# Kernel optimization log

Measured on AMD Instinct MI355X. Metric: run time of the kernel, lower is better.

## Reference

```python
import jax, jax.numpy as jnp
import numpy as np

N, E = 12288, 196608
IN_DIM, HID, HEADS, EMB, K = 128, 256, 4, 16, 2
NEG_SLOPE = 0.2


def gat_layer(x, src, dst, W, a_s, a_d, b, heads, out_dim):
    # x: [N, Fin]; src/dst: [E'] (self-loops already appended)
    n = x.shape[0]
    h = (x @ W).reshape(n, heads, out_dim)                 # [N,H,F]
    alpha_src = jnp.einsum('nhf,hf->nh', h, a_s)           # [N,H]
    alpha_dst = jnp.einsum('nhf,hf->nh', h, a_d)
    e = jax.nn.leaky_relu(alpha_src[src] + alpha_dst[dst], NEG_SLOPE)  # [E,H]
    # softmax over incoming edges per destination node
    m = jax.ops.segment_max(e, dst, num_segments=n)
    ex = jnp.exp(e - m[dst])
    s = jax.ops.segment_sum(ex, dst, num_segments=n)
    alpha = ex / s[dst]                                    # [E,H]
    msg = h[src] * alpha[..., None]                        # [E,H,F]
    agg = jax.ops.segment_sum(msg, dst, num_segments=n)    # [N,H,F]
    return agg.reshape(n, heads * out_dim) + b


def setup_inputs() -> dict:
    key = jax.random.key(0)
    ks = jax.random.split(key, 16)
    x = jax.random.normal(ks[0], (N, IN_DIM), dtype=jnp.float32)
    edge_index = jax.random.randint(ks[1], (2, E), 0, N, dtype=jnp.int32)

    def glorot(k, shape):
        fan = shape[0] + shape[-1]
        return jax.random.normal(k, shape, dtype=jnp.float32) * jnp.sqrt(2.0 / fan)

    inp = {"x": x, "edge_index": edge_index}
    inp["W1"] = glorot(ks[2], (IN_DIM, HEADS * HID))
    inp["as1"] = glorot(ks[3], (HEADS, HID))
    inp["ad1"] = glorot(ks[4], (HEADS, HID))
    inp["b1"] = jnp.zeros((HEADS * HID,), jnp.float32)
    inp["W2"] = glorot(ks[5], (HEADS * HID, HEADS * HID))
    inp["as2"] = glorot(ks[6], (HEADS, HID))
    inp["ad2"] = glorot(ks[7], (HEADS, HID))
    inp["b2"] = jnp.zeros((HEADS * HID,), jnp.float32)
    # layer 3: 1024 -> 16, 1 head
    inp["W3"] = glorot(ks[8], (HEADS * HID, EMB))
    inp["as3"] = glorot(ks[9], (1, EMB))
    inp["ad3"] = glorot(ks[10], (1, EMB))
    inp["b3"] = jnp.zeros((EMB,), jnp.float32)
    inp["centers"] = jax.random.normal(ks[11], (K, EMB), dtype=jnp.float32)
    return inp


def reference(x, edge_index, W1, as1, ad1, b1, W2, as2, ad2, b2, W3, as3, ad3, b3, centers):
    n = x.shape[0]
    loop = jnp.arange(n, dtype=edge_index.dtype)
    src = jnp.concatenate([edge_index[0], loop])
    dst = jnp.concatenate([edge_index[1], loop])

    h = jax.nn.elu(gat_layer(x, src, dst, W1, as1, ad1, b1, HEADS, HID))
    h = jax.nn.elu(gat_layer(h, src, dst, W2, as2, ad2, b2, HEADS, HID))
    z = gat_layer(h, src, dst, W3, as3, ad3, b3, 1, EMB)   # [N,EMB]

    adj_recon = jax.nn.sigmoid(z @ z.T)                    # [N,N]

    # Student-t soft assignment
    d2 = jnp.sum((z[:, None, :] - centers[None, :, :]) ** 2, axis=2)  # [N,K]
    q = 1.0 / (1.0 + d2)
    q = q / jnp.sum(q, axis=1, keepdims=True)
    return z, adj_recon, q
```

## Files before the change

kernel.cpp:

```cpp
#include <hip/hip_runtime.h>
#include <hip/hip_bf16.h>
#include <math.h>

#define N_NODES 12288
#define N_EDGES 196608
#define EP_EDGES (N_EDGES + N_NODES)
#define HEADS 4
#define HID 256
#define FDIM 1024
#define EMB 16
#define NEG_SLOPE 0.2f

typedef __attribute__((ext_vector_type(8))) short short8;
typedef __attribute__((ext_vector_type(4))) float f32x4;
typedef __attribute__((ext_vector_type(2))) float f32x2;

__device__ __forceinline__ unsigned short f2bf(float f) {
  unsigned int u = __float_as_uint(f);
  u = (u + 0x7FFFu + ((u >> 16) & 1u)) >> 16;
  return (unsigned short)u;
}
__device__ __forceinline__ float bf2f(unsigned short h) {
  return __uint_as_float(((unsigned int)h) << 16);
}

__device__ __forceinline__ void t_tile_hi(const float* __restrict__ W,
                                          unsigned short* __restrict__ Th,
                                          int K, int N, int k0, int n0,
                                          int t, float (*tile)[33]) {
  int rr = t >> 3, cc = (t & 7) * 4;
  float4 v = *reinterpret_cast<const float4*>(&W[(size_t)(k0 + rr) * N + n0 + cc]);
  tile[rr][cc + 0] = v.x; tile[rr][cc + 1] = v.y; tile[rr][cc + 2] = v.z; tile[rr][cc + 3] = v.w;
  __syncthreads();
  ushort4 h;
  h.x = f2bf(tile[cc + 0][rr]);
  h.y = f2bf(tile[cc + 1][rr]);
  h.z = f2bf(tile[cc + 2][rr]);
  h.w = f2bf(tile[cc + 3][rr]);
  *reinterpret_cast<ushort4*>(&Th[(size_t)(n0 + rr) * K + k0 + cc]) = h;
}

#define HIST_BLKS (EP_EDGES / 256)
__global__ __launch_bounds__(256) void k_hist_prep(const int* __restrict__ ei,
                                                   int* __restrict__ cnt,
                                                   const float* __restrict__ x,
                                                   unsigned short* __restrict__ xbf,
                                                   const float* __restrict__ W1,
                                                   unsigned short* __restrict__ w1tHi,
                                                   const float* __restrict__ W2,
                                                   unsigned short* __restrict__ w2tHi,
                                                   const float* __restrict__ as1,
                                                   const float* __restrict__ ad1,
                                                   float* __restrict__ wa,
                                                   const float* __restrict__ W3,
                                                   unsigned short* __restrict__ w3t) {
  __shared__ float tile[32][33];
  int b = blockIdx.x, t = threadIdx.x;
  if (b < HIST_BLKS) {
    int i = b * 256 + t;
    if (i < EP_EDGES) {
      int d = (i < N_EDGES) ? ei[N_EDGES + i] : (i - N_EDGES);
      atomicAdd(&cnt[d], 1);
    }
  } else if (b < HIST_BLKS + 1536) {
    int i = (b - HIST_BLKS) * 256 + t;
    float4 v = *reinterpret_cast<const float4*>(&x[(size_t)i * 4]);
    ushort4 h;
    h.x = f2bf(v.x); h.y = f2bf(v.y); h.z = f2bf(v.z); h.w = f2bf(v.w);
    *reinterpret_cast<ushort4*>(&xbf[(size_t)i * 4]) = h;
  } else if (b < HIST_BLKS + 1536 + 128) {
    int tt = b - HIST_BLKS - 1536;
    t_tile_hi(W1, w1tHi, 128, FDIM, (tt >> 5) * 32, (tt & 31) * 32, t, tile);
  } else if (b < HIST_BLKS + 1536 + 128 + 1024) {
    int tt = b - HIST_BLKS - 1536 - 128;
    t_tile_hi(W2, w2tHi, FDIM, FDIM, (tt >> 5) * 32, (tt & 31) * 32, t, tile);
  } else if (b == HIST_BLKS + 1536 + 128 + 1024) {
    for (int idx = t; idx < 1024; idx += 256) {
      int sd = idx >> 9, h = (idx >> 7) & 3, k = idx & 127;
      const float* av = sd ? ad1 : as1;
      float acc = 0.f;
      for (int f = 0; f < 256; ++f)
        acc = fmaf(W1[(size_t)k * FDIM + h * 256 + f], av[h * 256 + f], acc);
      wa[idx] = acc;
    }
  } else {
    for (int idx = t; idx < 16384; idx += 256) {
      int c = idx >> 10, k = idx & 1023;
      w3t[idx] = f2bf(W3[(size_t)k * 16 + c]);
    }
  }
}

__global__ __launch_bounds__(1024) void k_scan_alpha(const int* __restrict__ cnt,
                                                     int* __restrict__ row_ptr,
                                                     int* __restrict__ bsum,
                                                     const float* __restrict__ x,
                                                     const float* __restrict__ wa,
                                                     float* __restrict__ asrc,
                                                     float* __restrict__ adst) {
  __shared__ int sd[1024];
  int tid = threadIdx.x;
  if (blockIdx.x < 12) {
    int gid = blockIdx.x * 1024 + tid;
    int v = cnt[gid];
    sd[tid] = v;
    __syncthreads();
    for (int d = 1; d < 1024; d <<= 1) {
      int t2 = (tid >= d) ? sd[tid - d] : 0;
      __syncthreads();
      sd[tid] += t2;
      __syncthreads();
    }
    row_ptr[gid] = sd[tid] - v;
    if (tid == 1023) bsum[blockIdx.x] = sd[1023];
  } else {
    int id = (blockIdx.x - 12) * 1024 + tid;
    int n = id >> 2, h = id & 3;
    const float* wsv = wa + h * 128;
    const float* wdv = wa + 512 + h * 128;
    const float* xr = x + (size_t)n * 128;
    float accs = 0.f, accd = 0.f;
#pragma unroll
    for (int k = 0; k < 128; k += 4) {
      float4 xv = *reinterpret_cast<const float4*>(&xr[k]);
      float4 s4 = *reinterpret_cast<const float4*>(&wsv[k]);
      float4 d4 = *reinterpret_cast<const float4*>(&wdv[k]);
      accs = fmaf(xv.x, s4.x, fmaf(xv.y, s4.y, fmaf(xv.z, s4.z, fmaf(xv.w, s4.w, accs))));
      accd = fmaf(xv.x, d4.x, fmaf(xv.y, d4.y, fmaf(xv.z, d4.z, fmaf(xv.w, d4.w, accd))));
    }
    asrc[n * 4 + h] = accs;
    adst[n * 4 + h] = accd;
  }
}

__global__ void k_scan23(int* __restrict__ row_ptr, const int* __restrict__ bsum) {
  int gid = blockIdx.x * 256 + threadIdx.x;
  int blk = gid >> 10;
  int boffv = 0;
  for (int j = 0; j < blk; ++j) boffv += bsum[j];
  row_ptr[gid] += boffv;
  if (gid == 0) {
    int tot = 0;
    for (int j = 0; j < 12; ++j) tot += bsum[j];
    row_ptr[N_NODES] = tot;
  }
}

__global__ void k_scatter(const int* __restrict__ ei, const int* __restrict__ row_ptr,
                          int* __restrict__ cur, int* __restrict__ csr_src) {
  int i = blockIdx.x * 256 + threadIdx.x;
  if (i >= EP_EDGES) return;
  int s, d;
  if (i < N_EDGES) { s = ei[i]; d = ei[N_EDGES + i]; }
  else             { s = i - N_EDGES; d = s; }
  int pos = row_ptr[d] + atomicAdd(&cur[d], 1);
  csr_src[pos] = s;
}

__global__ __launch_bounds__(256) void k_aggx(const unsigned short* __restrict__ xbf,
                                              const float* __restrict__ asrc,
                                              const float* __restrict__ adst,
                                              const int* __restrict__ row_ptr,
                                              const int* __restrict__ csr_src,
                                              unsigned short* __restrict__ outHi) {
  int node = (blockIdx.x * 256 + threadIdx.x) >> 6;
  int lane = threadIdx.x & 63;
  int beg = row_ptr[node], end = row_ptr[node + 1];
  float4 adn = *reinterpret_cast<const float4*>(&adst[node * 4]);
  float m0 = -INFINITY, m1 = -INFINITY, m2 = -INFINITY, m3 = -INFINITY;
  float s0 = 0.f, s1 = 0.f, s2 = 0.f, s3 = 0.f;
  float a0x = 0.f, a0y = 0.f, a1x = 0.f, a1y = 0.f;
  float a2x = 0.f, a2y = 0.f, a3x = 0.f, a3y = 0.f;
  for (int e = beg; e < end; ++e) {
    int sidx = csr_src[e];
    float4 av = *reinterpret_cast<const float4*>(&asrc[sidx * 4]);
    ushort2 hu = *reinterpret_cast<const ushort2*>(&xbf[(size_t)sidx * 128 + lane * 2]);
    float hx = bf2f(hu.x), hy = bf2f(hu.y);
    float a, nm, sc, p;
    a = av.x + adn.x; a = a > 0.f ? a : NEG_SLOPE * a;
    nm = fmaxf(m0, a); sc = __expf(m0 - nm); p = __expf(a - nm); m0 = nm;
    s0 = s0 * sc + p; a0x = a0x * sc + p * hx; a0y = a0y * sc + p * hy;
    a = av.y + adn.y; a = a > 0.f ? a : NEG_SLOPE * a;
    nm = fmaxf(m1, a); sc = __expf(m1 - nm); p = __expf(a - nm); m1 = nm;
    s1 = s1 * sc + p; a1x = a1x * sc + p * hx; a1y = a1y * sc + p * hy;
    a = av.z + adn.z; a = a > 0.f ? a : NEG_SLOPE * a;
    nm = fmaxf(m2, a); sc = __expf(m2 - nm); p = __expf(a - nm); m2 = nm;
    s2 = s2 * sc + p; a2x = a2x * sc + p * hx; a2y = a2y * sc + p * hy;
    a = av.w + adn.w; a = a > 0.f ? a : NEG_SLOPE * a;
    nm = fmaxf(m3, a); sc = __expf(m3 - nm); p = __expf(a - nm); m3 = nm;
    s3 = s3 * sc + p; a3x = a3x * sc + p * hx; a3y = a3y * sc + p * hy;
  }
  size_t base = (size_t)node * 512 + lane * 2;
  ushort2 o;
  float inv;
  inv = 1.f / s0; o.x = f2bf(a0x * inv); o.y = f2bf(a0y * inv);
  *reinterpret_cast<ushort2*>(&outHi[base + 0 * 128]) = o;
  inv = 1.f / s1; o.x = f2bf(a1x * inv); o.y = f2bf(a1y * inv);
  *reinterpret_cast<ushort2*>(&outHi[base + 1 * 128]) = o;
  inv = 1.f / s2; o.x = f2bf(a2x * inv); o.y = f2bf(a2y * inv);
  *reinterpret_cast<ushort2*>(&outHi[base + 2 * 128]) = o;
  inv = 1.f / s3; o.x = f2bf(a3x * inv); o.y = f2bf(a3y * inv);
  *reinterpret_cast<ushort2*>(&outHi[base + 3 * 128]) = o;
}

template <int MODE>
__global__ __launch_bounds__(256) void k_gemm(const unsigned short* __restrict__ A,
                                              const unsigned short* __restrict__ B,
                                              unsigned short* __restrict__ Out,
                                              const float* __restrict__ bias,
                                              const float* __restrict__ a_s,
                                              const float* __restrict__ a_d,
                                              float* __restrict__ asrcP,
                                              float* __restrict__ adstP,
                                              int M, int N, int K, int lda) {
  __shared__ unsigned short sA[128 * 32], sB[128 * 32];
  const int tid = threadIdx.x;
  const int lane = tid & 63, wv = tid >> 6;
  const int row0 = blockIdx.y * 128, col0 = blockIdx.x * 128;
  const int mBase = (wv >> 1) * 64, nBase = (wv & 1) * 64;
  const int lane15 = lane & 15;
  const int aoff = (MODE == 1) ? (col0 >> 8) * 128 : 0;

  f32x4 acc[4][4];
#pragma unroll
  for (int m = 0; m < 4; ++m)
#pragma unroll
    for (int n = 0; n < 4; ++n) acc[m][n] = (f32x4){0.f, 0.f, 0.f, 0.f};

  int rS[2], cS[2], dS[2];
#pragma unroll
  for (int c = 0; c < 2; ++c) {
    int p = c * 4096 + tid * 16;
    int r = p >> 6, u = (p >> 4) & 3;
    int f = (r & 3) ^ ((r >> 2) & 3);
    rS[c] = r; cS[c] = (u ^ f) * 8; dS[c] = c * 2048 + tid * 8;
  }
  const int fR = (lane & 3) ^ ((lane >> 2) & 3);
  const int uprime = (((lane >> 4) ^ fR) * 8);

  for (int k0 = 0; k0 < K; k0 += 32) {
#pragma unroll
    for (int c = 0; c < 2; ++c) {
      size_t ga = (size_t)(row0 + rS[c]) * lda + aoff + k0 + cS[c];
      size_t gb = (size_t)(col0 + rS[c]) * K + k0 + cS[c];
      __builtin_amdgcn_global_load_lds((const __attribute__((address_space(1))) void*)(A + ga),
                                       (__attribute__((address_space(3))) void*)(sA + dS[c]), 16, 0, 0);
      __builtin_amdgcn_global_load_lds((const __attribute__((address_space(1))) void*)(B + gb),
                                       (__attribute__((address_space(3))) void*)(sB + dS[c]), 16, 0, 0);
    }
    __syncthreads();

    short8 a[4], b[4];
#pragma unroll
    for (int m = 0; m < 4; ++m) {
      int ia = (mBase + m * 16 + lane15) * 32 + uprime;
      a[m] = *reinterpret_cast<const short8*>(sA + ia);
      int ib = (nBase + m * 16 + lane15) * 32 + uprime;
      b[m] = *reinterpret_cast<const short8*>(sB + ib);
    }
#pragma unroll
    for (int m = 0; m < 4; ++m)
#pragma unroll
      for (int n = 0; n < 4; ++n)
        acc[m][n] = __builtin_amdgcn_mfma_f32_16x16x32_bf16(a[m], b[n], acc[m][n], 0, 0, 0);
    __syncthreads();
  }

  const int head = col0 >> 8;
  const int q = ((col0 >> 6) & 2) | (nBase >> 6);
  float asv[4], adv[4];
  if (MODE == 0) {
#pragma unroll
    for (int n = 0; n < 4; ++n) {
      int cc = col0 + nBase + n * 16 + lane15;
      asv[n] = a_s[cc];
      adv[n] = a_d[cc];
    }
  }

#pragma unroll
  for (int m = 0; m < 4; ++m) {
    int rr = row0 + mBase + m * 16 + (lane >> 4) * 4;
#pragma unroll
    for (int j = 0; j < 4; ++j) {
      if (MODE == 1) {
#pragma unroll
        for (int n = 0; n < 4; ++n) {
          int cc = col0 + nBase + n * 16 + lane15;
          float v = acc[m][n][j] + bias[cc];
          v = v > 0.f ? v : __expf(v) - 1.f;
          Out[(size_t)(rr + j) * N + cc] = f2bf(v);
        }
      } else {
        float ps = 0.f, pd = 0.f;
#pragma unroll
        for (int n = 0; n < 4; ++n) {
          int cc = col0 + nBase + n * 16 + lane15;
          float v = acc[m][n][j];
          Out[(size_t)(rr + j) * N + cc] = f2bf(v);
          ps = fmaf(v, asv[n], ps);
          pd = fmaf(v, adv[n], pd);
        }
        ps += __shfl_xor(ps, 1); pd += __shfl_xor(pd, 1);
        ps += __shfl_xor(ps, 2); pd += __shfl_xor(pd, 2);
        ps += __shfl_xor(ps, 4); pd += __shfl_xor(pd, 4);
        ps += __shfl_xor(ps, 8); pd += __shfl_xor(pd, 8);
        if (lane15 == 0) {
          asrcP[(size_t)(rr + j) * 16 + head * 4 + q] = ps;
          adstP[(size_t)(rr + j) * 16 + head * 4 + q] = pd;
        }
      }
    }
  }
}

__global__ void k_repack8(const unsigned short* __restrict__ hbf,
                          unsigned int* __restrict__ h8) {
  int i = blockIdx.x * 256 + threadIdx.x;
  ushort4 v = *reinterpret_cast<const ushort4*>(&hbf[(size_t)i * 4]);
  int w = __builtin_amdgcn_cvt_pk_fp8_f32(bf2f(v.x), bf2f(v.y), 0, false);
  w = __builtin_amdgcn_cvt_pk_fp8_f32(bf2f(v.z), bf2f(v.w), w, true);
  h8[i] = (unsigned int)w;
}

__global__ __launch_bounds__(256) void k_agg4(const unsigned int* __restrict__ h8,
                                              const float* __restrict__ asrcP,
                                              const float* __restrict__ adstP,
                                              const int* __restrict__ row_ptr,
                                              const int* __restrict__ csr_src, const float* __restrict__ bias,
                                              unsigned short* __restrict__ outHi) {
  int wid = (blockIdx.x * 256 + threadIdx.x) >> 6;
  int lane = threadIdx.x & 63;
  int node = wid >> 2, hd = wid & 3;
  int beg = row_ptr[node], end = row_ptr[node + 1];
  float4 dq = *reinterpret_cast<const float4*>(&adstP[(size_t)node * 16 + hd * 4]);
  float adn = dq.x + dq.y + dq.z + dq.w;
  float m = -INFINITY, s = 0.f;
  float ax = 0.f, ay = 0.f, az = 0.f, aw = 0.f;
  for (int e = beg; e < end; ++e) {
    int sidx = csr_src[e];
    float4 sq = *reinterpret_cast<const float4*>(&asrcP[(size_t)sidx * 16 + hd * 4]);
    float a = (sq.x + sq.y + sq.z + sq.w) + adn;
    a = a > 0.f ? a : NEG_SLOPE * a;
    float nm = fmaxf(m, a);
    float sc = __expf(m - nm);
    float p  = __expf(a - nm);
    m = nm;
    s = s * sc + p;
    unsigned int dw = h8[(size_t)sidx * 256 + hd * 64 + lane];
    f32x2 lo = __builtin_amdgcn_cvt_pk_f32_fp8(dw, false);
    f32x2 hi = __builtin_amdgcn_cvt_pk_f32_fp8(dw, true);
    ax = ax * sc + p * lo.x;
    ay = ay * sc + p * lo.y;
    az = az * sc + p * hi.x;
    aw = aw * sc + p * hi.y;
  }
  float inv = 1.f / s;
  int fo = hd * HID + lane * 4;
  float4 bv = *reinterpret_cast<const float4*>(&bias[fo]);
  float4 o;
  o.x = ax * inv + bv.x; o.y = ay * inv + bv.y; o.z = az * inv + bv.z; o.w = aw * inv + bv.w;
  o.x = o.x > 0.f ? o.x : __expf(o.x) - 1.f;
  o.y = o.y > 0.f ? o.y : __expf(o.y) - 1.f;
  o.z = o.z > 0.f ? o.z : __expf(o.z) - 1.f;
  o.w = o.w > 0.f ? o.w : __expf(o.w) - 1.f;
  ushort4 hh;
  hh.x = f2bf(o.x); hh.y = f2bf(o.y); hh.z = f2bf(o.z); hh.w = f2bf(o.w);
  *reinterpret_cast<ushort4*>(&outHi[(size_t)node * FDIM + fo]) = hh;
}

__global__ __launch_bounds__(256) void k_gemm_n16(const unsigned short* __restrict__ A,
                                                  const unsigned short* __restrict__ w3t,
                                                  const float* __restrict__ a_s,
                                                  const float* __restrict__ a_d,
                                                  float* __restrict__ C,
                                                  float* __restrict__ asrc,
                                                  float* __restrict__ adst) {
  int wave = (blockIdx.x * 256 + threadIdx.x) >> 6;
  int lane = threadIdx.x & 63;
  int lane15 = lane & 15;
  int row0 = wave * 16;
  int kg = (lane >> 4) * 8;
  f32x4 acc = (f32x4){0.f, 0.f, 0.f, 0.f};
  const unsigned short* Ar = A + (size_t)(row0 + lane15) * FDIM + kg;
  const unsigned short* Br = w3t + (size_t)lane15 * FDIM + kg;
  for (int k0 = 0; k0 < FDIM; k0 += 32) {
    short8 a = *reinterpret_cast<const short8*>(Ar + k0);
    short8 b = *reinterpret_cast<const short8*>(Br + k0);
    acc = __builtin_amdgcn_mfma_f32_16x16x32_bf16(a, b, acc, 0, 0, 0);
  }
  float asv = a_s[lane15], adv = a_d[lane15];
  int rbase = row0 + (lane >> 4) * 4;
#pragma unroll
  for (int j = 0; j < 4; ++j) {
    float v = acc[j];
    C[(size_t)(rbase + j) * EMB + lane15] = v;
    float ps = v * asv, pd = v * adv;
    ps += __shfl_xor(ps, 1); pd += __shfl_xor(pd, 1);
    ps += __shfl_xor(ps, 2); pd += __shfl_xor(pd, 2);
    ps += __shfl_xor(ps, 4); pd += __shfl_xor(pd, 4);
    ps += __shfl_xor(ps, 8); pd += __shfl_xor(pd, 8);
    if (lane15 == 0) { asrc[rbase + j] = ps; adst[rbase + j] = pd; }
  }
}

__global__ __launch_bounds__(256) void k_agg1(const float* __restrict__ h3, const float* __restrict__ asrc,
                                              const float* __restrict__ adst, const int* __restrict__ row_ptr,
                                              const int* __restrict__ csr_src, const float* __restrict__ bias,
                                              const float* __restrict__ centers,
                                              float* __restrict__ z, float* __restrict__ qout,
                                              unsigned short* __restrict__ zh,
                                              unsigned short* __restrict__ zl) {
  int idx = blockIdx.x * 256 + threadIdx.x;
  int node = idx >> 4, f = idx & 15;
  if (node >= N_NODES) return;
  int beg = row_ptr[node], end = row_ptr[node + 1];
  float adn = adst[node];
  float m = -INFINITY, s = 0.f, acc = 0.f;
  for (int e = beg; e < end; ++e) {
    int sidx = csr_src[e];
    float a = asrc[sidx] + adn;
    a = a > 0.f ? a : NEG_SLOPE * a;
    float nm = fmaxf(m, a);
    float sc = __expf(m - nm);
    float p  = __expf(a - nm);
    m = nm;
    s = s * sc + p;
    acc = acc * sc + p * h3[sidx * EMB + f];
  }
  float zv = acc / s + bias[f];
  z[node * EMB + f] = zv;
  unsigned short hv = f2bf(zv);
  zh[node * EMB + f] = hv;
  zl[node * EMB + f] = f2bf(zv - bf2f(hv));
  float d0 = zv - centers[f];       d0 *= d0;
  float d1 = zv - centers[EMB + f]; d1 *= d1;
  d0 += __shfl_xor(d0, 1); d1 += __shfl_xor(d1, 1);
  d0 += __shfl_xor(d0, 2); d1 += __shfl_xor(d1, 2);
  d0 += __shfl_xor(d0, 4); d1 += __shfl_xor(d1, 4);
  d0 += __shfl_xor(d0, 8); d1 += __shfl_xor(d1, 8);
  if (f == 0) {
    float q0 = 1.f / (1.f + d0), q1 = 1.f / (1.f + d1);
    float inv = 1.f / (q0 + q1);
    qout[node * 2 + 0] = q0 * inv;
    qout[node * 2 + 1] = q1 * inv;
  }
}

__global__ __launch_bounds__(256) void k_adj(const unsigned short* __restrict__ zh,
                                             const unsigned short* __restrict__ zl,
                                             float* __restrict__ adj) {
  int tid = threadIdx.x;
  int lane = tid & 63, wv = tid >> 6;
  int r0 = blockIdx.y * 128 + wv * 32, c0 = blockIdx.x * 128;
  int l15 = lane & 15, kg = lane >> 4;
  short8 zero = (short8){0, 0, 0, 0, 0, 0, 0, 0};
  short8 ah[2], al[2];
#pragma unroll
  for (int g = 0; g < 2; ++g) {
    int row = r0 + g * 16 + l15;
    if (kg < 2) {
      ah[g] = *reinterpret_cast<const short8*>(&zh[(size_t)row * EMB + kg * 8]);
      al[g] = *reinterpret_cast<const short8*>(&zl[(size_t)row * EMB + kg * 8]);
    } else { ah[g] = zero; al[g] = zero; }
  }
  short8 bh[8], bl[8];
#pragma unroll
  for (int n = 0; n < 8; ++n) {
    int col = c0 + n * 16 + l15;
    if (kg < 2) {
      bh[n] = *reinterpret_cast<const short8*>(&zh[(size_t)col * EMB + kg * 8]);
      bl[n] = *reinterpret_cast<const short8*>(&zl[(size_t)col * EMB + kg * 8]);
    } else { bh[n] = zero; bl[n] = zero; }
  }
#pragma unroll
  for (int g = 0; g < 2; ++g) {
    int rbase = r0 + g * 16 + kg * 4;
#pragma unroll
    for (int n = 0; n < 8; ++n) {
      f32x4 acc = (f32x4){0.f, 0.f, 0.f, 0.f};
      acc = __builtin_amdgcn_mfma_f32_16x16x32_bf16(ah[g], bh[n], acc, 0, 0, 0);
      acc = __builtin_amdgcn_mfma_f32_16x16x32_bf16(ah[g], bl[n], acc, 0, 0, 0);
      acc = __builtin_amdgcn_mfma_f32_16x16x32_bf16(al[g], bh[n], acc, 0, 0, 0);
      int cc = c0 + n * 16 + l15;
#pragma unroll
      for (int j = 0; j < 4; ++j) {
        float v = 1.f / (1.f + __expf(-acc[j]));
        adj[(size_t)(rbase + j) * N_NODES + cc] = v;
      }
    }
  }
}

extern "C" void kernel_launch(void* const* d_in, const int* in_sizes, int n_in,
                              void* d_out, int out_size, void* d_ws, size_t ws_size,
                              hipStream_t stream) {
  const float* x   = (const float*)d_in[0];
  const int*   ei  = (const int*)d_in[1];
  const float* W1  = (const float*)d_in[2];
  const float* as1 = (const float*)d_in[3];
  const float* ad1 = (const float*)d_in[4];
  const float* b1  = (const float*)d_in[5];
  const float* W2  = (const float*)d_in[6];
  const float* as2 = (const float*)d_in[7];
  const float* ad2 = (const float*)d_in[8];
  const float* b2  = (const float*)d_in[9];
  const float* W3  = (const float*)d_in[10];
  const float* as3 = (const float*)d_in[11];
  const float* ad3 = (const float*)d_in[12];
  const float* b3  = (const float*)d_in[13];
  const float* centers = (const float*)d_in[14];
  float* out = (float*)d_out;

  char* ws = (char*)d_ws;
  size_t off = 0;
  auto alloc = [&](size_t bytes) { void* p = ws + off; off = (off + bytes + 255) & ~(size_t)255; return p; };
  int* cnt       = (int*)alloc((size_t)N_NODES * 4);
  int* cur       = (int*)alloc((size_t)N_NODES * 4);
  int* row_ptr   = (int*)alloc((size_t)(N_NODES + 1) * 4);
  int* bsum      = (int*)alloc(64 * 4);
  int* csr_src   = (int*)alloc((size_t)EP_EDGES * 4);
  float* asrcA   = (float*)alloc((size_t)N_NODES * HEADS * 4);
  float* adstA   = (float*)alloc((size_t)N_NODES * HEADS * 4);
  float* asrcP   = (float*)alloc((size_t)N_NODES * 16 * 4);
  float* adstP   = (float*)alloc((size_t)N_NODES * 16 * 4);
  float* asrc3   = (float*)alloc((size_t)N_NODES * 4);
  float* adst3   = (float*)alloc((size_t)N_NODES * 4);
  float* wa      = (float*)alloc(1024 * 4);
  unsigned short* xbf    = (unsigned short*)alloc((size_t)N_NODES * 128 * 2);
  unsigned short* aggxHi = (unsigned short*)alloc((size_t)N_NODES * 512 * 2);
  unsigned short* h1bf   = (unsigned short*)alloc((size_t)N_NODES * FDIM * 2);
  unsigned short* hbf    = (unsigned short*)alloc((size_t)N_NODES * FDIM * 2);
  unsigned int*   h8     = (unsigned int*)alloc((size_t)N_NODES * FDIM);
  unsigned short* agg2Hi = (unsigned short*)alloc((size_t)N_NODES * FDIM * 2);
  unsigned short* w1tHi  = (unsigned short*)alloc((size_t)FDIM * 128 * 2);
  unsigned short* w2tHi  = (unsigned short*)alloc((size_t)FDIM * FDIM * 2);
  unsigned short* w3t    = (unsigned short*)alloc((size_t)16 * FDIM * 2);
  unsigned short* zh     = (unsigned short*)alloc((size_t)N_NODES * EMB * 2);
  unsigned short* zl     = (unsigned short*)alloc((size_t)N_NODES * EMB * 2);
  float* bufZ    = (float*)alloc((size_t)N_NODES * EMB * 4);

  hipMemsetAsync(cnt, 0, (size_t)N_NODES * 8, stream);

  k_hist_prep<<<dim3(HIST_BLKS + 1536 + 128 + 1024 + 2), dim3(256), 0, stream>>>(
      ei, cnt, x, xbf, W1, w1tHi, W2, w2tHi, as1, ad1, wa, W3, w3t);

  k_scan_alpha<<<dim3(12 + 48), dim3(1024), 0, stream>>>(
      cnt, row_ptr, bsum, x, wa, asrcA, adstA);

  k_scan23<<<dim3(N_NODES / 256), dim3(256), 0, stream>>>(row_ptr, bsum);
  k_scatter<<<dim3((EP_EDGES + 255) / 256), dim3(256), 0, stream>>>(ei, row_ptr, cur, csr_src);

  k_aggx<<<dim3(N_NODES / 4), dim3(256), 0, stream>>>(xbf, asrcA, adstA, row_ptr, csr_src, aggxHi);
  k_gemm<1><<<dim3(FDIM / 128, N_NODES / 128), dim3(256), 0, stream>>>(
      aggxHi, w1tHi, h1bf, b1, nullptr, nullptr, nullptr, nullptr, N_NODES, FDIM, 128, 512);

  k_gemm<0><<<dim3(FDIM / 128, N_NODES / 128), dim3(256), 0, stream>>>(
      h1bf, w2tHi, hbf, nullptr, as2, ad2, asrcP, adstP, N_NODES, FDIM, FDIM, FDIM);
  k_repack8<<<dim3(N_NODES * FDIM / 4 / 256), dim3(256), 0, stream>>>(hbf, h8);
  k_agg4<<<dim3(N_NODES), dim3(256), 0, stream>>>(h8, asrcP, adstP, row_ptr, csr_src, b2, agg2Hi);

  k_gemm_n16<<<dim3(N_NODES / 64), dim3(256), 0, stream>>>(
      agg2Hi, w3t, as3, ad3, bufZ, asrc3, adst3);
  float* adj = out + (size_t)N_NODES * EMB;
  float* q   = adj + (size_t)N_NODES * N_NODES;
  k_agg1<<<dim3(N_NODES * EMB / 256), dim3(256), 0, stream>>>(
      bufZ, asrc3, adst3, row_ptr, csr_src, b3, centers, out, q, zh, zl);

  k_adj<<<dim3(N_NODES / 128, N_NODES / 128), dim3(256), 0, stream>>>(zh, zl, adj);
}
```

Measured before the change: 441.2 us.

## Fuse FP8 packing into GEMM epilogue and use two-pass softmax in aggregations

The layer-2 GEMM epilogue now shuffles accumulator values across lanes and writes FP8-packed words directly. This removes the separate bf16 output buffer and the repack kernel, saving a full write and re-read of the 12288x1024 hidden matrix. The three aggregation kernels replace online softmax with a two-pass scheme: a max pass over the edges, then a pass with one exp per edge and no rescaling. The trade-off is extra index and attention-logit gathers per edge, in exchange for fewer exps and shorter dependency chains.

New measurement: 494.1 us. 12.0% more time.

```diff
diff --git a/kernel.cpp b/kernel.cpp
--- a/kernel.cpp
+++ b/kernel.cpp
@@ -168,6 +168,15 @@
   int beg = row_ptr[node], end = row_ptr[node + 1];
   float4 adn = *reinterpret_cast<const float4*>(&adst[node * 4]);
   float m0 = -INFINITY, m1 = -INFINITY, m2 = -INFINITY, m3 = -INFINITY;
+  for (int e = beg; e < end; ++e) {
+    int sidx = csr_src[e];
+    float4 av = *reinterpret_cast<const float4*>(&asrc[sidx * 4]);
+    float a;
+    a = av.x + adn.x; a = a > 0.f ? a : NEG_SLOPE * a; m0 = fmaxf(m0, a);
+    a = av.y + adn.y; a = a > 0.f ? a : NEG_SLOPE * a; m1 = fmaxf(m1, a);
+    a = av.z + adn.z; a = a > 0.f ? a : NEG_SLOPE * a; m2 = fmaxf(m2, a);
+    a = av.w + adn.w; a = a > 0.f ? a : NEG_SLOPE * a; m3 = fmaxf(m3, a);
+  }
   float s0 = 0.f, s1 = 0.f, s2 = 0.f, s3 = 0.f;
   float a0x = 0.f, a0y = 0.f, a1x = 0.f, a1y = 0.f;
   float a2x = 0.f, a2y = 0.f, a3x = 0.f, a3y = 0.f;
@@ -176,19 +185,15 @@
     float4 av = *reinterpret_cast<const float4*>(&asrc[sidx * 4]);
     ushort2 hu = *reinterpret_cast<const ushort2*>(&xbf[(size_t)sidx * 128 + lane * 2]);
     float hx = bf2f(hu.x), hy = bf2f(hu.y);
-    float a, nm, sc, p;
+    float a, p;
     a = av.x + adn.x; a = a > 0.f ? a : NEG_SLOPE * a;
-    nm = fmaxf(m0, a); sc = __expf(m0 - nm); p = __expf(a - nm); m0 = nm;
-    s0 = s0 * sc + p; a0x = a0x * sc + p * hx; a0y = a0y * sc + p * hy;
+    p = __expf(a - m0); s0 += p; a0x = fmaf(p, hx, a0x); a0y = fmaf(p, hy, a0y);
     a = av.y + adn.y; a = a > 0.f ? a : NEG_SLOPE * a;
-    nm = fmaxf(m1, a); sc = __expf(m1 - nm); p = __expf(a - nm); m1 = nm;
-    s1 = s1 * sc + p; a1x = a1x * sc + p * hx; a1y = a1y * sc + p * hy;
+    p = __expf(a - m1); s1 += p; a1x = fmaf(p, hx, a1x); a1y = fmaf(p, hy, a1y);
     a = av.z + adn.z; a = a > 0.f ? a : NEG_SLOPE * a;
-    nm = fmaxf(m2, a); sc = __expf(m2 - nm); p = __expf(a - nm); m2 = nm;
-    s2 = s2 * sc + p; a2x = a2x * sc + p * hx; a2y = a2y * sc + p * hy;
+    p = __expf(a - m2); s2 += p; a2x = fmaf(p, hx, a2x); a2y = fmaf(p, hy, a2y);
     a = av.w + adn.w; a = a > 0.f ? a : NEG_SLOPE * a;
-    nm = fmaxf(m3, a); sc = __expf(m3 - nm); p = __expf(a - nm); m3 = nm;
-    s3 = s3 * sc + p; a3x = a3x * sc + p * hx; a3y = a3y * sc + p * hy;
+    p = __expf(a - m3); s3 += p; a3x = fmaf(p, hx, a3x); a3y = fmaf(p, hy, a3y);
   }
   size_t base = (size_t)node * 512 + lane * 2;
   ushort2 o;
@@ -206,7 +211,8 @@
 template <int MODE>
 __global__ __launch_bounds__(256) void k_gemm(const unsigned short* __restrict__ A,
                                               const unsigned short* __restrict__ B,
-                                              unsigned short* __restrict__ Out,
+                                              unsigned short* __restrict__ OutBf,
+                                              unsigned int* __restrict__ Out8,
                                               const float* __restrict__ bias,
                                               const float* __restrict__ a_s,
                                               const float* __restrict__ a_d,
@@ -289,15 +295,13 @@
           int cc = col0 + nBase + n * 16 + lane15;
           float v = acc[m][n][j] + bias[cc];
           v = v > 0.f ? v : __expf(v) - 1.f;
-          Out[(size_t)(rr + j) * N + cc] = f2bf(v);
+          OutBf[(size_t)(rr + j) * N + cc] = f2bf(v);
         }
       } else {
         float ps = 0.f, pd = 0.f;
 #pragma unroll
         for (int n = 0; n < 4; ++n) {
-          int cc = col0 + nBase + n * 16 + lane15;
           float v = acc[m][n][j];
-          Out[(size_t)(rr + j) * N + cc] = f2bf(v);
           ps = fmaf(v, asv[n], ps);
           pd = fmaf(v, adv[n], pd);
         }
@@ -309,18 +313,22 @@
           asrcP[(size_t)(rr + j) * 16 + head * 4 + q] = ps;
           adstP[(size_t)(rr + j) * 16 + head * 4 + q] = pd;
         }
+        int src = (lane & 48) | ((lane15 << 2) & 15);
+        float c0 = 0.f, c1 = 0.f, c2 = 0.f, c3 = 0.f;
+#pragma unroll
+        for (int nn = 0; nn < 4; ++nn) {
+          float t0 = __shfl(acc[m][nn][j], src + 0);
+          float t1 = __shfl(acc[m][nn][j], src + 1);
+          float t2 = __shfl(acc[m][nn][j], src + 2);
+          float t3 = __shfl(acc[m][nn][j], src + 3);
+          if ((lane15 >> 2) == nn) { c0 = t0; c1 = t1; c2 = t2; c3 = t3; }
+        }
+        int w = __builtin_amdgcn_cvt_pk_fp8_f32(c0, c1, 0, false);
+        w = __builtin_amdgcn_cvt_pk_fp8_f32(c2, c3, w, true);
+        Out8[(size_t)(rr + j) * (N >> 2) + ((col0 + nBase) >> 2) + lane15] = (unsigned int)w;
       }
     }
   }
-}
-
-__global__ void k_repack8(const unsigned short* __restrict__ hbf,
-                          unsigned int* __restrict__ h8) {
-  int i = blockIdx.x * 256 + threadIdx.x;
-  ushort4 v = *reinterpret_cast<const ushort4*>(&hbf[(size_t)i * 4]);
-  int w = __builtin_amdgcn_cvt_pk_fp8_f32(bf2f(v.x), bf2f(v.y), 0, false);
-  w = __builtin_amdgcn_cvt_pk_fp8_f32(bf2f(v.z), bf2f(v.w), w, true);
-  h8[i] = (unsigned int)w;
 }
 
 __global__ __launch_bounds__(256) void k_agg4(const unsigned int* __restrict__ h8,
@@ -335,25 +343,29 @@
   int beg = row_ptr[node], end = row_ptr[node + 1];
   float4 dq = *reinterpret_cast<const float4*>(&adstP[(size_t)node * 16 + hd * 4]);
   float adn = dq.x + dq.y + dq.z + dq.w;
-  float m = -INFINITY, s = 0.f;
-  float ax = 0.f, ay = 0.f, az = 0.f, aw = 0.f;
+  float m = -INFINITY;
   for (int e = beg; e < end; ++e) {
     int sidx = csr_src[e];
     float4 sq = *reinterpret_cast<const float4*>(&asrcP[(size_t)sidx * 16 + hd * 4]);
     float a = (sq.x + sq.y + sq.z + sq.w) + adn;
     a = a > 0.f ? a : NEG_SLOPE * a;
-    float nm = fmaxf(m, a);
-    float sc = __expf(m - nm);
-    float p  = __expf(a - nm);
-    m = nm;
-    s = s * sc + p;
+    m = fmaxf(m, a);
+  }
+  float s = 0.f, ax = 0.f, ay = 0.f, az = 0.f, aw = 0.f;
+  for (int e = beg; e < end; ++e) {
+    int sidx = csr_src[e];
+    float4 sq = *reinterpret_cast<const float4*>(&asrcP[(size_t)sidx * 16 + hd * 4]);
+    float a = (sq.x + sq.y + sq.z + sq.w) + adn;
+    a = a > 0.f ? a : NEG_SLOPE * a;
+    float p = __expf(a - m);
     unsigned int dw = h8[(size_t)sidx * 256 + hd * 64 + lane];
     f32x2 lo = __builtin_amdgcn_cvt_pk_f32_fp8(dw, false);
     f32x2 hi = __builtin_amdgcn_cvt_pk_f32_fp8(dw, true);
-    ax = ax * sc + p * lo.x;
-    ay = ay * sc + p * lo.y;
-    az = az * sc + p * hi.x;
-    aw = aw * sc + p * hi.y;
+    s += p;
+    ax = fmaf(p, lo.x, ax);
+    ay = fmaf(p, lo.y, ay);
+    az = fmaf(p, hi.x, az);
+    aw = fmaf(p, hi.y, aw);
   }
   float inv = 1.f / s;
   int fo = hd * HID + lane * 4;
@@ -416,17 +428,20 @@
   if (node >= N_NODES) return;
   int beg = row_ptr[node], end = row_ptr[node + 1];
   float adn = adst[node];
-  float m = -INFINITY, s = 0.f, acc = 0.f;
+  float m = -INFINITY;
+  for (int e = beg; e < end; ++e) {
+    float a = asrc[csr_src[e]] + adn;
+    a = a > 0.f ? a : NEG_SLOPE * a;
+    m = fmaxf(m, a);
+  }
+  float s = 0.f, acc = 0.f;
   for (int e = beg; e < end; ++e) {
     int sidx = csr_src[e];
     float a = asrc[sidx] + adn;
     a = a > 0.f ? a : NEG_SLOPE * a;
-    float nm = fmaxf(m, a);
-    float sc = __expf(m - nm);
-    float p  = __expf(a - nm);
-    m = nm;
-    s = s * sc + p;
-    acc = acc * sc + p * h3[sidx * EMB + f];
+    float p = __expf(a - m);
+    s += p;
+    acc = fmaf(p, h3[sidx * EMB + f], acc);
   }
   float zv = acc / s + bias[f];
   z[node * EMB + f] = zv;
@@ -530,7 +545,6 @@
   unsigned short* xbf    = (unsigned short*)alloc((size_t)N_NODES * 128 * 2);
   unsigned short* aggxHi = (unsigned short*)alloc((size_t)N_NODES * 512 * 2);
   unsigned short* h1bf   = (unsigned short*)alloc((size_t)N_NODES * FDIM * 2);
-  unsigned short* hbf    = (unsigned short*)alloc((size_t)N_NODES * FDIM * 2);
   unsigned int*   h8     = (unsigned int*)alloc((size_t)N_NODES * FDIM);
   unsigned short* agg2Hi = (unsigned short*)alloc((size_t)N_NODES * FDIM * 2);
   unsigned short* w1tHi  = (unsigned short*)alloc((size_t)FDIM * 128 * 2);
@@ -553,11 +567,10 @@
 
   k_aggx<<<dim3(N_NODES / 4), dim3(256), 0, stream>>>(xbf, asrcA, adstA, row_ptr, csr_src, aggxHi);
   k_gemm<1><<<dim3(FDIM / 128, N_NODES / 128), dim3(256), 0, stream>>>(
-      aggxHi, w1tHi, h1bf, b1, nullptr, nullptr, nullptr, nullptr, N_NODES, FDIM, 128, 512);
+      aggxHi, w1tHi, h1bf, nullptr, b1, nullptr, nullptr, nullptr, nullptr, N_NODES, FDIM, 128, 512);
 
   k_gemm<0><<<dim3(FDIM / 128, N_NODES / 128), dim3(256), 0, stream>>>(
-      h1bf, w2tHi, hbf, nullptr, as2, ad2, asrcP, adstP, N_NODES, FDIM, FDIM, FDIM);
-  k_repack8<<<dim3(N_NODES * FDIM / 4 / 256), dim3(256), 0, stream>>>(hbf, h8);
+      h1bf, w2tHi, nullptr, h8, nullptr, as2, ad2, asrcP, adstP, N_NODES, FDIM, FDIM, FDIM);
   k_agg4<<<dim3(N_NODES), dim3(256), 0, stream>>>(h8, asrcP, adstP, row_ptr, csr_src, b2, agg2Hi);
 
   k_gemm_n16<<<dim3(N_NODES / 64), dim3(256), 0, stream>>>(
```

## Process one node per wavefront in layer-2 aggregation with wide fp8 loads

Applied to the files above, without the earlier changes.

The layer-2 aggregation kernel now assigns one wavefront per node covering all four heads, with each lane loading 16 fp8 features as a uint4 instead of one dword per head-wave. Each edge's csr_src index and row pointer are therefore read once per node rather than four times. The repack kernel also pre-reduces the partial attention scores into per-node, per-head arrays, so the edge loop does a scalar load instead of a float4 load and sum. In exchange each lane carries 16 accumulators, which raises register pressure, and the edge loop runs 4x fewer waves, exposing less parallelism to hide gather latency.

Result: faster. 391.9 us (-11.2%).

```diff
diff --git a/kernel.cpp b/kernel.cpp
--- a/kernel.cpp
+++ b/kernel.cpp
@@ -315,58 +315,80 @@
 }
 
 __global__ void k_repack8(const unsigned short* __restrict__ hbf,
-                          unsigned int* __restrict__ h8) {
-  int i = blockIdx.x * 256 + threadIdx.x;
-  ushort4 v = *reinterpret_cast<const ushort4*>(&hbf[(size_t)i * 4]);
-  int w = __builtin_amdgcn_cvt_pk_fp8_f32(bf2f(v.x), bf2f(v.y), 0, false);
-  w = __builtin_amdgcn_cvt_pk_fp8_f32(bf2f(v.z), bf2f(v.w), w, true);
-  h8[i] = (unsigned int)w;
+                          unsigned int* __restrict__ h8,
+                          const float* __restrict__ asrcP,
+                          const float* __restrict__ adstP,
+                          float* __restrict__ asrcR,
+                          float* __restrict__ adstR) {
+  int b = blockIdx.x;
+  if (b < 12288) {
+    int i = b * 256 + threadIdx.x;
+    ushort4 v = *reinterpret_cast<const ushort4*>(&hbf[(size_t)i * 4]);
+    int w = __builtin_amdgcn_cvt_pk_fp8_f32(bf2f(v.x), bf2f(v.y), 0, false);
+    w = __builtin_amdgcn_cvt_pk_fp8_f32(bf2f(v.z), bf2f(v.w), w, true);
+    h8[i] = (unsigned int)w;
+  } else {
+    int i = (b - 12288) * 256 + threadIdx.x;
+    float4 sq = *reinterpret_cast<const float4*>(&asrcP[(size_t)i * 4]);
+    asrcR[i] = sq.x + sq.y + sq.z + sq.w;
+    float4 dq = *reinterpret_cast<const float4*>(&adstP[(size_t)i * 4]);
+    adstR[i] = dq.x + dq.y + dq.z + dq.w;
+  }
 }
 
 __global__ __launch_bounds__(256) void k_agg4(const unsigned int* __restrict__ h8,
-                                              const float* __restrict__ asrcP,
-                                              const float* __restrict__ adstP,
+                                              const float* __restrict__ asrcR,
+                                              const float* __restrict__ adstR,
                                               const int* __restrict__ row_ptr,
                                               const int* __restrict__ csr_src, const float* __restrict__ bias,
                                               unsigned short* __restrict__ outHi) {
-  int wid = (blockIdx.x * 256 + threadIdx.x) >> 6;
+  int node = (blockIdx.x * 256 + threadIdx.x) >> 6;
   int lane = threadIdx.x & 63;
-  int node = wid >> 2, hd = wid & 3;
+  int hd = lane >> 4;
   int beg = row_ptr[node], end = row_ptr[node + 1];
-  float4 dq = *reinterpret_cast<const float4*>(&adstP[(size_t)node * 16 + hd * 4]);
-  float adn = dq.x + dq.y + dq.z + dq.w;
+  float adn = adstR[node * 4 + hd];
   float m = -INFINITY, s = 0.f;
-  float ax = 0.f, ay = 0.f, az = 0.f, aw = 0.f;
+  float acc[16];
+#pragma unroll
+  for (int k = 0; k < 16; ++k) acc[k] = 0.f;
   for (int e = beg; e < end; ++e) {
     int sidx = csr_src[e];
-    float4 sq = *reinterpret_cast<const float4*>(&asrcP[(size_t)sidx * 16 + hd * 4]);
-    float a = (sq.x + sq.y + sq.z + sq.w) + adn;
+    float a = asrcR[sidx * 4 + hd] + adn;
     a = a > 0.f ? a : NEG_SLOPE * a;
     float nm = fmaxf(m, a);
     float sc = __expf(m - nm);
     float p  = __expf(a - nm);
     m = nm;
     s = s * sc + p;
-    unsigned int dw = h8[(size_t)sidx * 256 + hd * 64 + lane];
-    f32x2 lo = __builtin_amdgcn_cvt_pk_f32_fp8(dw, false);
-    f32x2 hi = __builtin_amdgcn_cvt_pk_f32_fp8(dw, true);
-    ax = ax * sc + p * lo.x;
-    ay = ay * sc + p * lo.y;
-    az = az * sc + p * hi.x;
-    aw = aw * sc + p * hi.y;
+    uint4 dw = *reinterpret_cast<const uint4*>(h8 + (size_t)sidx * 256 + lane * 4);
+#pragma unroll
+    for (int d = 0; d < 4; ++d) {
+      unsigned int w = (&dw.x)[d];
+      f32x2 lo = __builtin_amdgcn_cvt_pk_f32_fp8(w, false);
+      f32x2 hi = __builtin_amdgcn_cvt_pk_f32_fp8(w, true);
+      acc[d * 4 + 0] = acc[d * 4 + 0] * sc + p * lo.x;
+      acc[d * 4 + 1] = acc[d * 4 + 1] * sc + p * lo.y;
+      acc[d * 4 + 2] = acc[d * 4 + 2] * sc + p * hi.x;
+      acc[d * 4 + 3] = acc[d * 4 + 3] * sc + p * hi.y;
+    }
   }
   float inv = 1.f / s;
-  int fo = hd * HID + lane * 4;
-  float4 bv = *reinterpret_cast<const float4*>(&bias[fo]);
-  float4 o;
-  o.x = ax * inv + bv.x; o.y = ay * inv + bv.y; o.z = az * inv + bv.z; o.w = aw * inv + bv.w;
-  o.x = o.x > 0.f ? o.x : __expf(o.x) - 1.f;
-  o.y = o.y > 0.f ? o.y : __expf(o.y) - 1.f;
-  o.z = o.z > 0.f ? o.z : __expf(o.z) - 1.f;
-  o.w = o.w > 0.f ? o.w : __expf(o.w) - 1.f;
-  ushort4 hh;
-  hh.x = f2bf(o.x); hh.y = f2bf(o.y); hh.z = f2bf(o.z); hh.w = f2bf(o.w);
-  *reinterpret_cast<ushort4*>(&outHi[(size_t)node * FDIM + fo]) = hh;
+  int fo = lane * 16;
+#pragma unroll
+  for (int d = 0; d < 4; ++d) {
+    float4 bv = *reinterpret_cast<const float4*>(&bias[fo + d * 4]);
+    float v0 = acc[d * 4 + 0] * inv + bv.x;
+    float v1 = acc[d * 4 + 1] * inv + bv.y;
+    float v2 = acc[d * 4 + 2] * inv + bv.z;
+    float v3 = acc[d * 4 + 3] * inv + bv.w;
+    v0 = v0 > 0.f ? v0 : __expf(v0) - 1.f;
+    v1 = v1 > 0.f ? v1 : __expf(v1) - 1.f;
+    v2 = v2 > 0.f ? v2 : __expf(v2) - 1.f;
+    v3 = v3 > 0.f ? v3 : __expf(v3) - 1.f;
+    ushort4 st;
+    st.x = f2bf(v0); st.y = f2bf(v1); st.z = f2bf(v2); st.w = f2bf(v3);
+    *reinterpret_cast<ushort4*>(&outHi[(size_t)node * FDIM + fo + d * 4]) = st;
+  }
 }
 
 __global__ __launch_bounds__(256) void k_gemm_n16(const unsigned short* __restrict__ A,
@@ -524,6 +546,8 @@
   float* adstA   = (float*)alloc((size_t)N_NODES * HEADS * 4);
   float* asrcP   = (float*)alloc((size_t)N_NODES * 16 * 4);
   float* adstP   = (float*)alloc((size_t)N_NODES * 16 * 4);
+  float* asrcR   = (float*)alloc((size_t)N_NODES * 4 * 4);
+  float* adstR   = (float*)alloc((size_t)N_NODES * 4 * 4);
   float* asrc3   = (float*)alloc((size_t)N_NODES * 4);
   float* adst3   = (float*)alloc((size_t)N_NODES * 4);
   float* wa      = (float*)alloc(1024 * 4);
@@ -557,8 +581,9 @@
 
   k_gemm<0><<<dim3(FDIM / 128, N_NODES / 128), dim3(256), 0, stream>>>(
       h1bf, w2tHi, hbf, nullptr, as2, ad2, asrcP, adstP, N_NODES, FDIM, FDIM, FDIM);
-  k_repack8<<<dim3(N_NODES * FDIM / 4 / 256), dim3(256), 0, stream>>>(hbf, h8);
-  k_agg4<<<dim3(N_NODES), dim3(256), 0, stream>>>(h8, asrcP, adstP, row_ptr, csr_src, b2, agg2Hi);
+  k_repack8<<<dim3(12288 + N_NODES * 4 / 256), dim3(256), 0, stream>>>(
+      hbf, h8, asrcP, adstP, asrcR, adstR);
+  k_agg4<<<dim3(N_NODES / 4), dim3(256), 0, stream>>>(h8, asrcR, adstR, row_ptr, csr_src, b2, agg2Hi);
 
   k_gemm_n16<<<dim3(N_NODES / 64), dim3(256), 0, stream>>>(
       agg2Hi, w3t, as3, ad3, bufZ, asrc3, adst3);
```
